# Optimization experiments

Hardware: AMD Instinct MI355X
Metric: run time of the kernel (lower is better)

The kernel has to match this reference:

```python
import jax, jax.numpy as jnp
import numpy as np

RANK = 32
N_ITER = 10
H, W_DIM, C_DIM = 14, 14, 512  # input_shape = (h, w, c)


def _khatri_rao(X, Y):
    # X: [m, r], Y: [n, r] -> [m*n, r], row index = i*n + j (C-order)
    return (X[:, None, :] * Y[None, :, :]).reshape(X.shape[0] * Y.shape[0], X.shape[1])


def _parafac_als(T, key):
    """Rank-RANK CP/ALS decomposition of a single 3-way tensor T [c, h, w].

    Mirrors tensorly.parafac(..., n_iter_max=10, init='random') math:
    per-mode least-squares update factor_n = unfold_n(T) @ KR(others) @ pinv(gram hadamard).
    Returns factors (A [c,r], B [h,r], C [w,r]).
    """
    c, h, w = T.shape
    kA, kB, kC = jax.random.split(key, 3)
    A = jax.random.normal(kA, (c, RANK), dtype=T.dtype)
    B = jax.random.normal(kB, (h, RANK), dtype=T.dtype)
    C = jax.random.normal(kC, (w, RANK), dtype=T.dtype)

    T0 = T.reshape(c, h * w)                      # mode-0 unfolding
    T1 = jnp.transpose(T, (1, 0, 2)).reshape(h, c * w)  # mode-1 unfolding
    T2 = jnp.transpose(T, (2, 0, 1)).reshape(w, c * h)  # mode-2 unfolding

    for _ in range(N_ITER):
        A = T0 @ _khatri_rao(B, C) @ jnp.linalg.pinv((B.T @ B) * (C.T @ C))
        B = T1 @ _khatri_rao(A, C) @ jnp.linalg.pinv((A.T @ A) * (C.T @ C))
        C = T2 @ _khatri_rao(A, B) @ jnp.linalg.pinv((A.T @ A) * (B.T @ B))
    return A, B, C


def setup_inputs() -> dict:
    key = jax.random.key(0)
    k = jax.random.split(key, 5)
    batch = 64
    factor_len = RANK * (H + W_DIM + C_DIM)  # 17280
    hidden = factor_len // 2                 # 8640
    hash_len = 128
    x = jax.random.normal(k[0], (batch, C_DIM, H, W_DIM), dtype=jnp.float32)
    W1 = jax.random.normal(k[1], (hidden, factor_len), dtype=jnp.float32) * (1.0 / np.sqrt(factor_len))
    b1 = jnp.zeros((hidden,), dtype=jnp.float32)
    W2 = jax.random.normal(k[2], (hash_len, hidden), dtype=jnp.float32) * (1.0 / np.sqrt(hidden))
    b2 = jnp.zeros((hash_len,), dtype=jnp.float32)
    return {"x": x, "W1": W1, "b1": b1, "W2": W2, "b2": b2}


def reference(x, W1, b1, W2, b2):
    batch = x.shape[0]
    keys = jax.random.split(jax.random.key(42), batch)
    # batched per-sample CP/ALS (this replaces the Python loop over the batch)
    A, B, C = jax.vmap(_parafac_als)(x, keys)  # [B,c,r], [B,h,r], [B,w,r]
    factor_batch = jnp.concatenate(
        [A.reshape(batch, -1), B.reshape(batch, -1), C.reshape(batch, -1)], axis=1
    )  # [B, rank*(c+h+w)]
    h1 = jax.nn.relu(factor_batch @ W1.T + b1)
    continuous_hash = h1 @ W2.T + b2
    binary_hash = jnp.sign(continuous_hash)  # training STE collapses to sign in fwd
    return binary_hash, continuous_hash
```

## Files before the change

kernel.cpp:

```cpp
#include <hip/hip_runtime.h>
#include <stdint.h>
#include <math.h>

#define RANK 32
#define CDIM 512
#define HD   14
#define WD   14
#define HW   196
#define NITER 10
#define BATCH 64
#define FLEN 17280
#define HID  8640
#define HASH 128
#define NSWEEP 5
#define JSTR 34
#define NPOW_H 5
#define NPOW_I 6
#define KH   3
#define KSEG 5760
#define KT   90

#define A_OFF    0u
#define A_BYTES  8388608u
#define FB_OFF   8388608u
#define FB_BYTES 4423680u
#define BF_OFF   12812288u
#define CF_OFF   13041664u
#define GA_OFF   13271040u
#define P_OFF    13795328u
#define TA_OFF   14319616u
#define RES_OFF  15925248u
#define SENT_OFF 15926784u
#define NFB_OFF  15927040u
#define WS_NEED  15927044u
#define PART_OFF 0u
#define H1_OFF   GA_OFF

#define MAGIC_OK     0x5AFEC0DEu
#define MAGIC_RESBAD 0x0BAD0BADu

#define WSYNC() do { asm volatile("s_waitcnt lgkmcnt(0)" ::: "memory"); \
                     __builtin_amdgcn_wave_barrier(); } while (0)

__device__ __forceinline__ uint32_t rotl32(uint32_t x, int n) {
  return (x << n) | (x >> (32 - n));
}

__device__ __forceinline__ void tf2x32(uint32_t k0, uint32_t k1,
                                       uint32_t x0, uint32_t x1,
                                       uint32_t& y0, uint32_t& y1) {
  uint32_t ks2 = k0 ^ k1 ^ 0x1BD11BDAu;
  x0 += k0; x1 += k1;
#define TFRND(r) { x0 += x1; x1 = rotl32(x1, r); x1 ^= x0; }
  TFRND(13) TFRND(15) TFRND(26) TFRND(6)
  x0 += k1;  x1 += ks2 + 1u;
  TFRND(17) TFRND(29) TFRND(16) TFRND(24)
  x0 += ks2; x1 += k0 + 2u;
  TFRND(13) TFRND(15) TFRND(26) TFRND(6)
  x0 += k0;  x1 += k1 + 3u;
  TFRND(17) TFRND(29) TFRND(16) TFRND(24)
  x0 += k1;  x1 += ks2 + 4u;
  TFRND(13) TFRND(15) TFRND(26) TFRND(6)
  x0 += ks2; x1 += k0 + 5u;
#undef TFRND
  y0 = x0; y1 = x1;
}

__device__ __forceinline__ uint32_t pt_bits(uint32_t k0, uint32_t k1, uint32_t m) {
  uint32_t y0, y1;
  tf2x32(k0, k1, 0u, m, y0, y1);
  return y0 ^ y1;
}
__device__ __forceinline__ void pt_child(uint32_t k0, uint32_t k1, uint32_t i,
                                         uint32_t& c0, uint32_t& c1) {
  tf2x32(k0, k1, 0u, i, c0, c1);
}

__device__ __forceinline__ float erfinv_f32(float x) {
#pragma clang fp contract(off)
  float w = -log1pf(-x * x);
  float p;
  if (w < 5.0f) {
    w = w - 2.5f;
    p = 2.81022636e-08f;
    p = 3.43273939e-07f  + p * w;
    p = -3.5233877e-06f  + p * w;
    p = -4.39150654e-06f + p * w;
    p = 0.00021858087f   + p * w;
    p = -0.00125372503f  + p * w;
    p = -0.00417768164f  + p * w;
    p = 0.246640727f     + p * w;
    p = 1.50140941f      + p * w;
  } else {
    w = sqrtf(w) - 3.0f;
    p = -0.000200214257f;
    p = 0.000100950558f  + p * w;
    p = 0.00134934322f   + p * w;
    p = -0.00367342844f  + p * w;
    p = 0.00573950773f   + p * w;
    p = -0.0076224613f   + p * w;
    p = 0.00943887047f   + p * w;
    p = 1.00167406f      + p * w;
    p = 2.83297682f      + p * w;
  }
  return p * x;
}

__device__ __forceinline__ float nrm_val(uint32_t bits) {
#pragma clang fp contract(off)
  const float lo = -0.99999994f;
  float f = __uint_as_float((bits >> 9) | 0x3f800000u) - 1.0f;
  float u = fmaxf(lo, f * 2.0f + lo);
  return 1.41421356f * erfinv_f32(u);
}

__device__ __forceinline__ void derive_keys(int b,
    uint32_t& a0, uint32_t& a1, uint32_t& b0, uint32_t& b1, uint32_t& c0, uint32_t& c1) {
  uint32_t kb0, kb1;
  pt_child(0u, 42u, (uint32_t)b, kb0, kb1);
  pt_child(kb0, kb1, 0u, a0, a1);
  pt_child(kb0, kb1, 1u, b0, b1);
  pt_child(kb0, kb1, 2u, c0, c1);
}

__global__ __launch_bounds__(512) void init_kernel(double* __restrict__ A,
                                                   double* __restrict__ Bfac,
                                                   double* __restrict__ Cfac) {
  const int b = blockIdx.x, tid = threadIdx.x;
  uint32_t ka0, ka1, kb0, kb1, kc0, kc1;
  derive_keys(b, ka0, ka1, kb0, kb1, kc0, kc1);
  double* Ab = A + (size_t)b * CDIM * RANK;
  for (int m = tid; m < CDIM * RANK; m += 512)
    Ab[m] = (double)nrm_val(pt_bits(ka0, ka1, (uint32_t)m));
  for (int m = tid; m < HD * RANK; m += 512)
    Bfac[b * 448 + m] = (double)nrm_val(pt_bits(kb0, kb1, (uint32_t)m));
  for (int m = tid; m < WD * RANK; m += 512)
    Cfac[b * 448 + m] = (double)nrm_val(pt_bits(kc0, kc1, (uint32_t)m));
}

__device__ double powmax(const double* Hm, double* eigd, int lane, int n) {
  if (lane < 32) eigd[lane] = 1.0 + 0.001 * (double)lane;
  WSYNC();
  double mm = 0.0;
  for (int itp = 0; itp < n; ++itp) {
    double hv = 0.0;
    if (lane < 32) {
      const double* row = &Hm[lane * JSTR];
#pragma unroll 8
      for (int t = 0; t < 32; ++t) hv += row[t] * eigd[t];
    }
    mm = fabs(hv);
#pragma unroll
    for (int off = 1; off < 32; off <<= 1) mm = fmax(mm, __shfl_xor(mm, off));
    WSYNC();
    if (lane < 32) eigd[lane] = hv / mm;
    WSYNC();
  }
  return mm;
}

__device__ __forceinline__ void pq_of(int g, int rr, int& p, int& q) {
  if (g == 0) { p = 31; q = rr; }
  else { p = (rr + g) % 31; q = (rr - g + 31) % 31; }
}

__device__ void jacobi_wave(double* __restrict__ Hm, double* __restrict__ VT,
                            double* __restrict__ eigd, double* __restrict__ rc,
                            double* __restrict__ rs, int lane) {
  for (int e = lane; e < 32 * JSTR; e += 64) VT[e] = 0.0;
  WSYNC();
  if (lane < 32) VT[lane * JSTR + lane] = 1.0;
  WSYNC();
  const int g4   = lane >> 2;
  const int sub  = lane & 3;
  const int jr   = lane & 15;
  const int rowb = (lane >> 4) * 8;
  for (int sw = 0; sw < NSWEEP; ++sw) {
    for (int rr = 0; rr < 31; ++rr) {
      if (lane < 16) {
        int p, q; pq_of(lane, rr, p, q);
        double app = Hm[p * JSTR + p], aqq = Hm[q * JSTR + q], apq = Hm[p * JSTR + q];
        double c = 1.0, s = 0.0;
        if (fabs(apq) > 1e-300) {
          double tau = (aqq - app) / (2.0 * apq);
          double t = ((tau >= 0.0) ? 1.0 : -1.0) / (fabs(tau) + sqrt(1.0 + tau * tau));
          c = 1.0 / sqrt(1.0 + t * t);
          s = t * c;
        }
        rc[lane] = c; rs[lane] = s;
      }
      WSYNC();
      {
        int p, q; pq_of(g4, rr, p, q);
        const double c = rc[g4], s = rs[g4];
        double2* hp = (double2*)&Hm[p * JSTR + sub * 8];
        double2* hq = (double2*)&Hm[q * JSTR + sub * 8];
        double2* vp = (double2*)&VT[p * JSTR + sub * 8];
        double2* vq = (double2*)&VT[q * JSTR + sub * 8];
#pragma unroll
        for (int u = 0; u < 4; ++u) {
          double2 a = hp[u], bb = hq[u];
          hp[u] = make_double2(c * a.x - s * bb.x, c * a.y - s * bb.y);
          hq[u] = make_double2(s * a.x + c * bb.x, s * a.y + c * bb.y);
          double2 va = vp[u], vb = vq[u];
          vp[u] = make_double2(c * va.x - s * vb.x, c * va.y - s * vb.y);
          vq[u] = make_double2(s * va.x + c * vb.x, s * va.y + c * vb.y);
        }
      }
      WSYNC();
      {
        int p, q; pq_of(jr, rr, p, q);
        const double c = rc[jr], s = rs[jr];
#pragma unroll
        for (int u = 0; u < 8; ++u) {
          const int ro = (rowb + u) * JSTR;
          double a = Hm[ro + p], bb = Hm[ro + q];
          Hm[ro + p] = c * a - s * bb;
          Hm[ro + q] = s * a + c * bb;
        }
      }
      WSYNC();
    }
  }
  if (lane == 0) {
    double smax = 0.0;
    for (int i = 0; i < 32; ++i) smax = fmax(smax, fabs(Hm[i * JSTR + i]));
    const double cutoff = 3.814697265625e-05 * smax;
    for (int i = 0; i < 32; ++i) {
      double lam = Hm[i * JSTR + i];
      eigd[i] = (fabs(lam) > cutoff) ? 1.0 / lam : 0.0;
    }
  }
  WSYNC();
}

__device__ void build_H(int which, const double* Bs, const double* Cs,
                        const double* Gab, double* Hm, int lane) {
  for (int t = 0; t < 16; ++t) {
    int e = lane * 16 + t;
    int r1 = e >> 5, r2 = e & 31;
    double h;
    if (which == 0) {
      double sb = 0.0, sc = 0.0;
      for (int i = 0; i < HD; ++i) sb += Bs[i * RANK + r1] * Bs[i * RANK + r2];
      for (int j = 0; j < WD; ++j) sc += Cs[j * RANK + r1] * Cs[j * RANK + r2];
      h = sb * sc;
    } else if (which == 1) {
      double sc = 0.0;
      for (int j = 0; j < WD; ++j) sc += Cs[j * RANK + r1] * Cs[j * RANK + r2];
      h = Gab[e] * sc;
    } else {
      double sb = 0.0;
      for (int i = 0; i < HD; ++i) sb += Bs[i * RANK + r1] * Bs[i * RANK + r2];
      h = Gab[e] * sb;
    }
    Hm[r1 * JSTR + r2] = h;
  }
}

__device__ void pinv_wave_compute(int which, const double* Bs, const double* Cs,
                                  const double* Gab, double* Hm, double* VT,
                                  double* eigd, double* rcs, double* rss,
                                  int lane, unsigned int* nfb) {
  build_H(which, Bs, Cs, Gab, Hm, lane);
  WSYNC();
  double lamH = powmax(Hm, eigd, lane, NPOW_H);
  int bad = 0;
  const int col = lane & 31;
  const int r0  = (lane >> 5) * 16;
  for (int k = 0; k < 32; ++k) {
    double akk = Hm[k * JSTR + k];
    if (!(akk > 0.0)) bad = 1;
    double rk = 1.0 / akk;
    if (lane < 32) {
      double v = Hm[k * JSTR + lane];
      Hm[k * JSTR + lane] = (lane == k) ? rk : v * rk;
    }
    WSYNC();
    double pc = Hm[k * JSTR + col];
    for (int ii = 0; ii < 16; ++ii) {
      int i = r0 + ii;
      if (i == k) continue;
      double f  = Hm[i * JSTR + k];
      double ov = Hm[i * JSTR + col];
      Hm[i * JSTR + col] = (col == k) ? (-f * rk) : (ov - f * pc);
    }
    WSYNC();
  }
  double lamI = powmax(Hm, eigd, lane, NPOW_I);
  int ok = 0;
  if (lane == 0)
    ok = (!bad && (4.0 * 3.814697265625e-05 * lamH * lamI < 1.0)) ? 1 : 0;
  ok = __shfl(ok, 0);
  if (!ok) {
    build_H(which, Bs, Cs, Gab, Hm, lane);
    WSYNC();
    jacobi_wave(Hm, VT, eigd, rcs, rss, lane);
    for (int t = 0; t < 16; ++t) {
      int e = lane * 16 + t;
      int i = e >> 5, j = e & 31;
      double sacc = 0.0;
      for (int kk = 0; kk < 32; ++kk)
        sacc += eigd[kk] * VT[kk * JSTR + i] * VT[kk * JSTR + j];
      Hm[i * JSTR + j] = sacc;
    }
    WSYNC();
    if (lane == 0) atomicAdd(nfb, 1u);
  }
}

__global__ __launch_bounds__(512) void res_pinv_kernel(const float* __restrict__ x,
                                                       const double* __restrict__ A,
                                                       const double* __restrict__ Bfac,
                                                       const double* __restrict__ Cfac,
                                                       double* __restrict__ resbuf,
                                                       double* __restrict__ P,
                                                       unsigned int* __restrict__ nfb) {
  __shared__ float KR[HW * RANK];
  __shared__ double red[512];
  __shared__ double Hm[RANK * JSTR];
  __shared__ double VT[RANK * JSTR];
  __shared__ double Bs[HD * RANK];
  __shared__ double Cs[WD * RANK];
  __shared__ double eigd[RANK];
  __shared__ double rcs[16], rss[16];
  const int tid = threadIdx.x;

  if (blockIdx.x < BATCH) {
    const int b = blockIdx.x;
    const double* Bf = Bfac + b * 448;
    const double* Cf = Cfac + b * 448;
    const double* Ab = A + (size_t)b * CDIM * RANK;
    const float* T0 = x + (size_t)b * CDIM * HW;
    for (int e = tid; e < HW * RANK; e += 512) {
      int ij = e >> 5, r = e & 31;
      KR[e] = (float)(Bf[(ij / WD) * RANK + r] * Cf[(ij % WD) * RANK + r]);
    }
    __syncthreads();
    double areg[32];
    {
      const double2* ar2 = (const double2*)(Ab + (size_t)tid * RANK);
#pragma unroll
      for (int r2 = 0; r2 < 16; ++r2) {
        double2 v = ar2[r2];
        areg[r2 * 2] = v.x;
        areg[r2 * 2 + 1] = v.y;
      }
    }
    double rs = 0.0, nt = 0.0;
    const float4* Trow = (const float4*)(T0 + (size_t)tid * HW);
    for (int q4 = 0; q4 < HW / 4; ++q4) {
      float4 tv = Trow[q4];
#pragma unroll
      for (int u = 0; u < 4; ++u) {
        const int ij = q4 * 4 + u;
        const float4* kr4 = (const float4*)&KR[ij * RANK];
        double f = 0.0;
#pragma unroll
        for (int r4 = 0; r4 < 8; ++r4) {
          float4 kv = kr4[r4];
          f += areg[r4 * 4 + 0] * (double)kv.x;
          f += areg[r4 * 4 + 1] * (double)kv.y;
          f += areg[r4 * 4 + 2] * (double)kv.z;
          f += areg[r4 * 4 + 3] * (double)kv.w;
        }
        double tvd = (double)((const float*)&tv)[u];
        double d = tvd - f;
        rs += d * d; nt += tvd * tvd;
      }
    }
    red[tid] = rs;
    __syncthreads();
    for (int s = 256; s > 0; s >>= 1) {
      if (tid < s) red[tid] += red[tid + s];
      __syncthreads();
    }
    double rsum = red[0];
    __syncthreads();
    red[tid] = nt;
    __syncthreads();
    for (int s = 256; s > 0; s >>= 1) {
      if (tid < s) red[tid] += red[tid + s];
      __syncthreads();
    }
    if (tid == 0) { resbuf[b * 3] = rsum; resbuf[b * 3 + 1] = red[0]; }
  } else {
    const int b = blockIdx.x - BATCH;
    if (tid < 64) {
      const int lane = tid;
      for (int m = lane; m < HD * RANK; m += 64) Bs[m] = Bfac[b * 448 + m];
      for (int m = lane; m < WD * RANK; m += 64) Cs[m] = Cfac[b * 448 + m];
      WSYNC();
      pinv_wave_compute(0, Bs, Cs, nullptr, Hm, VT, eigd, rcs, rss, lane, nfb);
      for (int t = 0; t < 16; ++t) {
        int e = lane * 16 + t;
        P[b * 1024 + e] = Hm[(e >> 5) * JSTR + (e & 31)];
      }
    }
  }
}

__global__ __launch_bounds__(128) void updA_kernel(const float* __restrict__ x,
                                                   const double* __restrict__ Bfac,
                                                   const double* __restrict__ Cfac,
                                                   const double* __restrict__ P,
                                                   double* __restrict__ A) {
  __shared__ float KR[HW * RANK];
  __shared__ double Ps[1024];
  const int b = blockIdx.x >> 2, rb = blockIdx.x & 3;
  const int tid = threadIdx.x;
  const double* Bf = Bfac + b * 448;
  const double* Cf = Cfac + b * 448;
  for (int e = tid; e < HW * RANK; e += 128) {
    int ij = e >> 5, r = e & 31;
    KR[e] = (float)(Bf[(ij / WD) * RANK + r] * Cf[(ij % WD) * RANK + r]);
  }
  for (int e = tid; e < 1024; e += 128) Ps[e] = P[b * 1024 + e];
  __syncthreads();

  const int a = rb * 128 + tid;
  double acc[32];
#pragma unroll
  for (int r = 0; r < 32; ++r) acc[r] = 0.0;
  const float4* Trow = (const float4*)(x + (size_t)b * CDIM * HW + (size_t)a * HW);
  for (int q4 = 0; q4 < HW / 4; ++q4) {
    float4 tv = Trow[q4];
#pragma unroll
    for (int u = 0; u < 4; ++u) {
      double tvd = (double)((const float*)&tv)[u];
      const float4* kr4 = (const float4*)&KR[(q4 * 4 + u) * RANK];
#pragma unroll
      for (int r4 = 0; r4 < 8; ++r4) {
        float4 kv = kr4[r4];
        acc[r4 * 4 + 0] += tvd * (double)kv.x;
        acc[r4 * 4 + 1] += tvd * (double)kv.y;
        acc[r4 * 4 + 2] += tvd * (double)kv.z;
        acc[r4 * 4 + 3] += tvd * (double)kv.w;
      }
    }
  }
  double* Ab = A + (size_t)b * CDIM * RANK + (size_t)a * RANK;
  for (int r = 0; r < 32; ++r) {
    const double2* jrow = (const double2*)&Ps[r * 32];
    double s = 0.0;
#pragma unroll
    for (int k2 = 0; k2 < 16; ++k2) {
      double2 jv = jrow[k2];
      s += jv.x * acc[k2 * 2] + jv.y * acc[k2 * 2 + 1];
    }
    Ab[r] = s;
  }
}

__global__ __launch_bounds__(512) void ga_ta_kernel(const double* __restrict__ A,
                                                    const double* __restrict__ Cfac,
                                                    double* __restrict__ Ga,
                                                    double* __restrict__ P,
                                                    unsigned int* __restrict__ nfb,
                                                    const float* __restrict__ x,
                                                    float* __restrict__ TA) {
  __shared__ double Ach[64 * RANK];
  __shared__ double Gas[1024];
  __shared__ double Cs[WD * RANK];
  __shared__ double Hm[RANK * JSTR];
  __shared__ double VT[RANK * JSTR];
  __shared__ double eigd[RANK];
  __shared__ double rcs[16], rss[16];
  const int tid = threadIdx.x;

  if (blockIdx.x < BATCH) {
    const int b = blockIdx.x;
    const double* Ab = A + (size_t)b * CDIM * RANK;
    for (int m = tid; m < WD * RANK; m += 512) Cs[m] = Cfac[b * 448 + m];
    double g0 = 0.0, g1 = 0.0;
    const int r10 = tid >> 5, r20 = tid & 31;
    const int e1 = tid + 512;
    const int r11 = e1 >> 5, r21 = e1 & 31;
    for (int ch = 0; ch < CDIM / 64; ++ch) {
      for (int e = tid; e < 64 * RANK; e += 512) Ach[e] = Ab[ch * 64 * RANK + e];
      __syncthreads();
      for (int aa = 0; aa < 64; ++aa) {
        const double* ar = &Ach[aa * RANK];
        g0 += ar[r10] * ar[r20];
        g1 += ar[r11] * ar[r21];
      }
      __syncthreads();
    }
    Ga[b * 1024 + tid] = g0;  Gas[tid] = g0;
    Ga[b * 1024 + e1]  = g1;  Gas[e1]  = g1;
    __syncthreads();
    if (tid < 64) {
      pinv_wave_compute(1, nullptr, Cs, Gas, Hm, VT, eigd, rcs, rss, tid, nfb);
      for (int t = 0; t < 16; ++t) {
        int e = tid * 16 + t;
        P[b * 1024 + e] = Hm[(e >> 5) * JSTR + (e & 31)];
      }
    }
  } else {
    const int bb = blockIdx.x - BATCH;
    const int b = bb >> 2, r8 = bb & 3;
    const int ij = tid;
    if (ij >= HW) return;
    const float* T0 = x + (size_t)b * CDIM * HW;
    const double* Ab = A + (size_t)b * CDIM * RANK + r8 * 8;
    double ta[8];
#pragma unroll
    for (int r = 0; r < 8; ++r) ta[r] = 0.0;
    for (int a = 0; a < CDIM; ++a) {
      double tvd = (double)T0[(size_t)a * HW + ij];
      const double2* ap2 = (const double2*)(Ab + (size_t)a * RANK);
#pragma unroll
      for (int r2 = 0; r2 < 4; ++r2) {
        double2 av = ap2[r2];
        ta[r2 * 2]     += tvd * av.x;
        ta[r2 * 2 + 1] += tvd * av.y;
      }
    }
#pragma unroll
    for (int r = 0; r < 8; ++r)
      TA[b * 6272 + ij * RANK + r8 * 8 + r] = (float)ta[r];
  }
}

__global__ __launch_bounds__(512) void updB_pinv2_kernel(const float* __restrict__ TA,
                                                         const double* __restrict__ Cfac,
                                                         const double* __restrict__ Ga,
                                                         double* __restrict__ P,
                                                         double* __restrict__ Bfac,
                                                         unsigned int* __restrict__ nfb) {
  __shared__ double Mt[HD * RANK];
  __shared__ double Cs[WD * RANK];
  __shared__ double Bs[HD * RANK];
  __shared__ double Gas[1024];
  __shared__ double Hm[RANK * JSTR];
  __shared__ double VT[RANK * JSTR];
  __shared__ double eigd[RANK];
  __shared__ double rcs[16], rss[16];
  const int b = blockIdx.x, tid = threadIdx.x;
  const float* TAb = TA + b * 6272;
  for (int m = tid; m < WD * RANK; m += 512) Cs[m] = Cfac[b * 448 + m];
  for (int m = tid; m < 1024; m += 512) Gas[m] = Ga[b * 1024 + m];
  __syncthreads();
  if (tid < HD * RANK) {
    int i = tid >> 5, r = tid & 31;
    double s = 0.0;
    for (int j = 0; j < WD; ++j)
      s += (double)TAb[(i * WD + j) * RANK + r] * Cs[j * RANK + r];
    Mt[tid] = s;
  }
  __syncthreads();
  if (tid < HD) {
    const int i = tid;
    const double* Pb = P + b * 1024;
    for (int r = 0; r < 32; ++r) {
      const double2* jrow = (const double2*)&Pb[r * 32];
      const double2* mrow = (const double2*)&Mt[i * RANK];
      double s = 0.0;
#pragma unroll
      for (int k2 = 0; k2 < 16; ++k2) {
        double2 jv = jrow[k2]; double2 mv = mrow[k2];
        s += jv.x * mv.x + jv.y * mv.y;
      }
      Bs[i * RANK + r] = s;
      Bfac[b * 448 + i * RANK + r] = s;
    }
  }
  __syncthreads();
  if (tid < 64) {
    pinv_wave_compute(2, Bs, nullptr, Gas, Hm, VT, eigd, rcs, rss, tid, nfb);
    for (int t = 0; t < 16; ++t) {
      int e = tid * 16 + t;
      P[b * 1024 + e] = Hm[(e >> 5) * JSTR + (e & 31)];
    }
  }
}

__global__ __launch_bounds__(512) void updC_pinv0_kernel(const float* __restrict__ TA,
                                                         const double* __restrict__ Bfac,
                                                         double* __restrict__ P,
                                                         double* __restrict__ Cfac,
                                                         unsigned int* __restrict__ nfb,
                                                         int do_pinv) {
  __shared__ double Mt[WD * RANK];
  __shared__ double Bs[HD * RANK];
  __shared__ double Cs[WD * RANK];
  __shared__ double Hm[RANK * JSTR];
  __shared__ double VT[RANK * JSTR];
  __shared__ double eigd[RANK];
  __shared__ double rcs[16], rss[16];
  const int b = blockIdx.x, tid = threadIdx.x;
  const float* TAb = TA + b * 6272;
  for (int m = tid; m < HD * RANK; m += 512) Bs[m] = Bfac[b * 448 + m];
  __syncthreads();
  if (tid < WD * RANK) {
    int j = tid >> 5, r = tid & 31;
    double s = 0.0;
    for (int i = 0; i < HD; ++i)
      s += (double)TAb[(i * WD + j) * RANK + r] * Bs[i * RANK + r];
    Mt[tid] = s;
  }
  __syncthreads();
  if (tid < WD) {
    const int j = tid;
    const double* Pb = P + b * 1024;
    for (int r = 0; r < 32; ++r) {
      const double2* jrow = (const double2*)&Pb[r * 32];
      const double2* mrow = (const double2*)&Mt[j * RANK];
      double s = 0.0;
#pragma unroll
      for (int k2 = 0; k2 < 16; ++k2) {
        double2 jv = jrow[k2]; double2 mv = mrow[k2];
        s += jv.x * mv.x + jv.y * mv.y;
      }
      Cs[j * RANK + r] = s;
      Cfac[b * 448 + j * RANK + r] = s;
    }
  }
  __syncthreads();
  if (do_pinv && tid < 64) {
    pinv_wave_compute(0, Bs, Cs, nullptr, Hm, VT, eigd, rcs, rss, tid, nfb);
    for (int t = 0; t < 16; ++t) {
      int e = tid * 16 + t;
      P[b * 1024 + e] = Hm[(e >> 5) * JSTR + (e & 31)];
    }
  }
}

__global__ __launch_bounds__(512) void res_kernel(const float* __restrict__ x,
                                                  const double* __restrict__ A,
                                                  const double* __restrict__ Bfac,
                                                  const double* __restrict__ Cfac,
                                                  double* __restrict__ resbuf,
                                                  uint32_t* __restrict__ sent,
                                                  float* __restrict__ fb) {
  __shared__ float KR[HW * RANK];
  __shared__ double red[512];
  const int b = blockIdx.x, tid = threadIdx.x;
  const double* Bf = Bfac + b * 448;
  const double* Cf = Cfac + b * 448;
  const double* Ab = A + (size_t)b * CDIM * RANK;
  const float* T0 = x + (size_t)b * CDIM * HW;
  for (int e = tid; e < HW * RANK; e += 512) {
    int ij = e >> 5, r = e & 31;
    KR[e] = (float)(Bf[(ij / WD) * RANK + r] * Cf[(ij % WD) * RANK + r]);
  }
  __syncthreads();
  double areg[32];
  {
    const double2* ar2 = (const double2*)(Ab + (size_t)tid * RANK);
#pragma unroll
    for (int r2 = 0; r2 < 16; ++r2) {
      double2 v = ar2[r2];
      areg[r2 * 2] = v.x;
      areg[r2 * 2 + 1] = v.y;
    }
  }
  double rs = 0.0, nt = 0.0;
  const float4* Trow = (const float4*)(T0 + (size_t)tid * HW);
  for (int q4 = 0; q4 < HW / 4; ++q4) {
    float4 tv = Trow[q4];
#pragma unroll
    for (int u = 0; u < 4; ++u) {
      const int ij = q4 * 4 + u;
      const float4* kr4 = (const float4*)&KR[ij * RANK];
      double f = 0.0;
#pragma unroll
      for (int r4 = 0; r4 < 8; ++r4) {
        float4 kv = kr4[r4];
        f += areg[r4 * 4 + 0] * (double)kv.x;
        f += areg[r4 * 4 + 1] * (double)kv.y;
        f += areg[r4 * 4 + 2] * (double)kv.z;
        f += areg[r4 * 4 + 3] * (double)kv.w;
      }
      double tvd = (double)((const float*)&tv)[u];
      double d = tvd - f;
      rs += d * d; nt += tvd * tvd;
    }
  }
  red[tid] = rs;
  __syncthreads();
  for (int s = 256; s > 0; s >>= 1) {
    if (tid < s) red[tid] += red[tid + s];
    __syncthreads();
  }
  double rsum = red[0];
  __syncthreads();
  red[tid] = nt;
  __syncthreads();
  for (int s = 256; s > 0; s >>= 1) {
    if (tid < s) red[tid] += red[tid + s];
    __syncthreads();
  }
  double ntsum = red[0];
  (void)ntsum;

  if (tid == 0)
    sent[b] = (rsum < resbuf[b * 3] && rsum < resbuf[b * 3 + 1]) ? MAGIC_OK : MAGIC_RESBAD;
  float* fbb = fb + (size_t)b * FLEN;
  for (int m = tid; m < CDIM * RANK; m += 512) fbb[m] = (float)Ab[m];
  for (int m = tid; m < HD * RANK; m += 512)
    fbb[CDIM * RANK + m] = (float)Bf[m];
  for (int m = tid; m < WD * RANK; m += 512)
    fbb[CDIM * RANK + HD * RANK + m] = (float)Cf[m];
}

__global__ __launch_bounds__(256) void gemm1_kernel(const float* __restrict__ fb,
                                                    const float* __restrict__ W1,
                                                    float* __restrict__ part) {
  __shared__ __align__(16) float FBs[2][64][72];
  const int cb = blockIdx.x % 135;
  const int kh = blockIdx.x / 135;
  const int t  = threadIdx.x;
  const int cs = t >> 3;
  const int rg = t & 7;
  const int ca = cb * 64 + cs * 2;
  const int cb2 = ca + 1;
  const int srow = t >> 2;
  const int skk  = (t & 3) * 16;
  const int kh0 = kh * KSEG;
  float acc0[8], acc1[8];
#pragma unroll
  for (int r = 0; r < 8; ++r) { acc0[r] = 0.0f; acc1[r] = 0.0f; }

  const float4* src = (const float4*)(fb + (size_t)srow * FLEN + kh0 + skk);
  float4 s0 = src[0], s1 = src[1], s2 = src[2], s3 = src[3];
  int cur = 0;

  for (int kt = 0; kt < KT; ++kt) {
    float (*B)[72] = FBs[cur];
    B[skk + 0][srow]  = s0.x; B[skk + 1][srow]  = s0.y;
    B[skk + 2][srow]  = s0.z; B[skk + 3][srow]  = s0.w;
    B[skk + 4][srow]  = s1.x; B[skk + 5][srow]  = s1.y;
    B[skk + 6][srow]  = s1.z; B[skk + 7][srow]  = s1.w;
    B[skk + 8][srow]  = s2.x; B[skk + 9][srow]  = s2.y;
    B[skk + 10][srow] = s2.z; B[skk + 11][srow] = s2.w;
    B[skk + 12][srow] = s3.x; B[skk + 13][srow] = s3.y;
    B[skk + 14][srow] = s3.z; B[skk + 15][srow] = s3.w;
    __syncthreads();
    if (kt + 1 < KT) {
      src = (const float4*)(fb + (size_t)srow * FLEN + kh0 + (kt + 1) * 64 + skk);
      s0 = src[0]; s1 = src[1]; s2 = src[2]; s3 = src[3];
    }
    const int kbase = kh0 + kt * 64;
    const float4* wa = (const float4*)(W1 + (size_t)ca  * FLEN + kbase);
    const float4* wb = (const float4*)(W1 + (size_t)cb2 * FLEN + kbase);
    for (int k4 = 0; k4 < 16; ++k4) {
      float4 va = wa[k4], vb = wb[k4];
#pragma unroll
      for (int u = 0; u < 4; ++u) {
        const int k = k4 * 4 + u;
        const float fa = ((const float*)&va)[u];
        const float fbv = ((const float*)&vb)[u];
        const float4 f0 = *(const float4*)&B[k][rg * 8];
        const float4 f1 = *(const float4*)&B[k][rg * 8 + 4];
        const float fv[8] = { f0.x, f0.y, f0.z, f0.w, f1.x, f1.y, f1.z, f1.w };
#pragma unroll
        for (int r = 0; r < 8; ++r) {
          acc0[r] += fv[r] * fa;
          acc1[r] += fv[r] * fbv;
        }
      }
    }
    cur ^= 1;
  }
#pragma unroll
  for (int r = 0; r < 8; ++r) {
    const int row = rg * 8 + r;
    part[((size_t)kh * 64 + row) * HID + ca]  = acc0[r];
    part[((size_t)kh * 64 + row) * HID + cb2] = acc1[r];
  }
}

__global__ __launch_bounds__(256) void reduce_relu_kernel(const float* __restrict__ part,
                                                          const float* __restrict__ b1,
                                                          float* __restrict__ h1) {
  const int idx = blockIdx.x * 256 + threadIdx.x;
  if (idx < BATCH * HID) {
    const int col = idx % HID;
    const float v = part[idx] + part[BATCH * HID + idx] + part[2 * BATCH * HID + idx]
                  + b1[col];
    h1[idx] = fmaxf(v, 0.0f);
  }
}

__global__ __launch_bounds__(256) void gemm2_kernel(const float* __restrict__ h1,
                                                    const float* __restrict__ W2,
                                                    const float* __restrict__ b2,
                                                    const unsigned int* __restrict__ nfb,
                                                    float* __restrict__ out) {
  const int gid = blockIdx.x * 256 + threadIdx.x;
  const int bb = gid >> 7, o = gid & 127;
  const float4* hp = (const float4*)(h1 + (size_t)bb * HID);
  const float4* wp = (const float4*)(W2 + (size_t)o * HID);
  double acc = 0.0;
  for (int k4 = 0; k4 < HID / 4; ++k4) {
    float4 hv = hp[k4], wv = wp[k4];
    acc += (double)hv.x * (double)wv.x;
    acc += (double)hv.y * (double)wv.y;
    acc += (double)hv.z * (double)wv.z;
    acc += (double)hv.w * (double)wv.w;
  }
  const double cont = acc + (double)b2[o];
  const float cf = (float)cont;
  unsigned int nt = *nfb;
  const float jit = 2e-3f * (float)(nt < 8u ? nt : 8u);
  const float sg = (cf > 0.0f) ? 1.0f : ((cf < 0.0f) ? -1.0f : 0.0f);
  out[bb * HASH + o] = sg + jit;
  out[BATCH * HASH + bb * HASH + o] = cf;
}

__global__ __launch_bounds__(256) void diag_kernel(const uint32_t* __restrict__ sent,
                                                   float* __restrict__ out) {
  __shared__ int nmiss, nres, Vs;
  const int t = threadIdx.x;
  if (t == 0) { nmiss = 0; nres = 0; }
  __syncthreads();
  if (t < BATCH) {
    uint32_t s = sent[t];
    if (s == MAGIC_RESBAD) atomicAdd(&nres, 1);
    else if (s != MAGIC_OK) atomicAdd(&nmiss, 1);
  }
  __syncthreads();
  if (t == 0) {
    uint32_t y0, y1; int mask = 0;
    tf2x32(0u, 0u, 0u, 0u, y0, y1);
    if (y0 == 0x6b200159u && y1 == 0x99ba4efeu) mask |= 1;
    tf2x32(0xffffffffu, 0xffffffffu, 0xffffffffu, 0xffffffffu, y0, y1);
    if (y0 == 0x1cb996fcu && y1 == 0xbb002be7u) mask |= 2;
    tf2x32(0x13198a2eu, 0x03707344u, 0x243f6a88u, 0x85a308d3u, y0, y1);
    if (y0 == 0xc4923a9cu && y1 == 0x483df7a0u) mask |= 4;
    int V = 0;
    if (nmiss > 0) V = 30;
    else if (nres > 0) V = 40;
    else if (mask != 7) V = 10 + mask;
    Vs = V;
  }
  __syncthreads();
  const int V = Vs;
  if (V > 0) {
    for (int i = t; i < BATCH * HASH; i += 256) out[i] = (float)V;
  }
}

__global__ __launch_bounds__(256) void zero_out_kernel(float* __restrict__ out, int n) {
  const int idx = blockIdx.x * 256 + threadIdx.x;
  if (idx < n) out[idx] = 0.0f;
}

__global__ void init_ctr_kernel(unsigned int* __restrict__ ctr) {
  if (threadIdx.x == 0) *ctr = 0u;
}

extern "C" void kernel_launch(void* const* d_in, const int* in_sizes, int n_in,
                              void* d_out, int out_size, void* d_ws, size_t ws_size,
                              hipStream_t stream) {
  (void)in_sizes; (void)n_in;
  const float* x  = (const float*)d_in[0];
  const float* W1 = (const float*)d_in[1];
  const float* b1 = (const float*)d_in[2];
  const float* W2 = (const float*)d_in[3];
  const float* b2 = (const float*)d_in[4];
  float* out = (float*)d_out;

  if (ws_size < (size_t)WS_NEED) {
    hipLaunchKernelGGL(zero_out_kernel, dim3((out_size + 255) / 256), dim3(256), 0, stream,
                       out, out_size);
    return;
  }

  char* ws = (char*)d_ws;
  double*       A    = (double*)(ws + A_OFF);
  float*        fb   = (float*)(ws + FB_OFF);
  double*       Bfac = (double*)(ws + BF_OFF);
  double*       Cfac = (double*)(ws + CF_OFF);
  double*       Ga   = (double*)(ws + GA_OFF);
  double*       P    = (double*)(ws + P_OFF);
  float*        TA   = (float*)(ws + TA_OFF);
  double*       resb = (double*)(ws + RES_OFF);
  uint32_t*     sent = (uint32_t*)(ws + SENT_OFF);
  unsigned int* nfb  = (unsigned int*)(ws + NFB_OFF);
  float*        part = (float*)(ws + PART_OFF);
  float*        h1   = (float*)(ws + H1_OFF);

  hipLaunchKernelGGL(init_ctr_kernel, dim3(1), dim3(64), 0, stream, nfb);
  hipLaunchKernelGGL(init_kernel, dim3(BATCH), dim3(512), 0, stream, A, Bfac, Cfac);
  hipLaunchKernelGGL(res_pinv_kernel, dim3(2 * BATCH), dim3(512), 0, stream,
                     x, A, Bfac, Cfac, resb, P, nfb);
  for (int it = 0; it < NITER; ++it) {
    hipLaunchKernelGGL(updA_kernel, dim3(BATCH * 4), dim3(128), 0, stream,
                       x, Bfac, Cfac, P, A);
    hipLaunchKernelGGL(ga_ta_kernel, dim3(BATCH + BATCH * 4), dim3(512), 0, stream,
                       A, Cfac, Ga, P, nfb, x, TA);
    hipLaunchKernelGGL(updB_pinv2_kernel, dim3(BATCH), dim3(512), 0, stream,
                       TA, Cfac, Ga, P, Bfac, nfb);
    hipLaunchKernelGGL(updC_pinv0_kernel, dim3(BATCH), dim3(512), 0, stream,
                       TA, Bfac, P, Cfac, nfb, (it < NITER - 1) ? 1 : 0);
  }
  hipLaunchKernelGGL(res_kernel, dim3(BATCH), dim3(512), 0, stream,
                     x, A, Bfac, Cfac, resb, sent, fb);
  hipLaunchKernelGGL(gemm1_kernel, dim3(KH * 135), dim3(256), 0, stream, fb, W1, part);
  hipLaunchKernelGGL(reduce_relu_kernel, dim3((BATCH * HID) / 256), dim3(256), 0, stream,
                     part, b1, h1);
  hipLaunchKernelGGL(gemm2_kernel, dim3((BATCH * HASH) / 256), dim3(256), 0, stream,
                     h1, W2, b2, nfb, out);
  hipLaunchKernelGGL(diag_kernel, dim3(1), dim3(256), 0, stream, sent, out);
}
```

Before: 4.320 ms.

## Fuse B and C factor updates into one kernel; halve gemm1 columns per block

Merges the mode-1 (B) and mode-2 (C) ALS update kernels into a single per-sample kernel. The pinv result computed for the B update is kept in shared memory and reused directly for the C update, which removes one launch per iteration and a global round trip of P and B. Separately, gemm1 now computes one output column per thread instead of two, doubling the grid to 810 blocks. That raises parallelism but reloads the shared feature tile twice as often relative to the useful FMAs.

```diff
diff --git a/kernel.cpp b/kernel.cpp
--- a/kernel.cpp
+++ b/kernel.cpp
@@ -19,6 +19,7 @@
 #define KH   3
 #define KSEG 5760
 #define KT   90
+#define NCB  270
 
 #define A_OFF    0u
 #define A_BYTES  8388608u
@@ -522,12 +523,13 @@
   }
 }
 
-__global__ __launch_bounds__(512) void updB_pinv2_kernel(const float* __restrict__ TA,
-                                                         const double* __restrict__ Cfac,
-                                                         const double* __restrict__ Ga,
-                                                         double* __restrict__ P,
-                                                         double* __restrict__ Bfac,
-                                                         unsigned int* __restrict__ nfb) {
+__global__ __launch_bounds__(512) void updBC_kernel(const float* __restrict__ TA,
+                                                    double* __restrict__ Cfac,
+                                                    const double* __restrict__ Ga,
+                                                    double* __restrict__ P,
+                                                    double* __restrict__ Bfac,
+                                                    unsigned int* __restrict__ nfb,
+                                                    int do_pinv) {
   __shared__ double Mt[HD * RANK];
   __shared__ double Cs[WD * RANK];
   __shared__ double Bs[HD * RANK];
@@ -568,29 +570,10 @@
   __syncthreads();
   if (tid < 64) {
     pinv_wave_compute(2, Bs, nullptr, Gas, Hm, VT, eigd, rcs, rss, tid, nfb);
-    for (int t = 0; t < 16; ++t) {
-      int e = tid * 16 + t;
-      P[b * 1024 + e] = Hm[(e >> 5) * JSTR + (e & 31)];
-    }
-  }
-}
-
-__global__ __launch_bounds__(512) void updC_pinv0_kernel(const float* __restrict__ TA,
-                                                         const double* __restrict__ Bfac,
-                                                         double* __restrict__ P,
-                                                         double* __restrict__ Cfac,
-                                                         unsigned int* __restrict__ nfb,
-                                                         int do_pinv) {
-  __shared__ double Mt[WD * RANK];
-  __shared__ double Bs[HD * RANK];
-  __shared__ double Cs[WD * RANK];
-  __shared__ double Hm[RANK * JSTR];
-  __shared__ double VT[RANK * JSTR];
-  __shared__ double eigd[RANK];
-  __shared__ double rcs[16], rss[16];
-  const int b = blockIdx.x, tid = threadIdx.x;
-  const float* TAb = TA + b * 6272;
-  for (int m = tid; m < HD * RANK; m += 512) Bs[m] = Bfac[b * 448 + m];
+  }
+  __syncthreads();
+  for (int e = tid; e < 1024; e += 512)
+    Gas[e] = Hm[(e >> 5) * JSTR + (e & 31)];
   __syncthreads();
   if (tid < WD * RANK) {
     int j = tid >> 5, r = tid & 31;
@@ -602,9 +585,8 @@
   __syncthreads();
   if (tid < WD) {
     const int j = tid;
-    const double* Pb = P + b * 1024;
     for (int r = 0; r < 32; ++r) {
-      const double2* jrow = (const double2*)&Pb[r * 32];
+      const double2* jrow = (const double2*)&Gas[r * 32];
       const double2* mrow = (const double2*)&Mt[j * RANK];
       double s = 0.0;
 #pragma unroll
@@ -708,19 +690,18 @@
                                                     const float* __restrict__ W1,
                                                     float* __restrict__ part) {
   __shared__ __align__(16) float FBs[2][64][72];
-  const int cb = blockIdx.x % 135;
-  const int kh = blockIdx.x / 135;
+  const int cb = blockIdx.x % NCB;
+  const int kh = blockIdx.x / NCB;
   const int t  = threadIdx.x;
   const int cs = t >> 3;
   const int rg = t & 7;
-  const int ca = cb * 64 + cs * 2;
-  const int cb2 = ca + 1;
+  const int ca = cb * 32 + cs;
   const int srow = t >> 2;
   const int skk  = (t & 3) * 16;
   const int kh0 = kh * KSEG;
-  float acc0[8], acc1[8];
-#pragma unroll
-  for (int r = 0; r < 8; ++r) { acc0[r] = 0.0f; acc1[r] = 0.0f; }
+  float acc0[8];
+#pragma unroll
+  for (int r = 0; r < 8; ++r) acc0[r] = 0.0f;
 
   const float4* src = (const float4*)(fb + (size_t)srow * FLEN + kh0 + skk);
   float4 s0 = src[0], s1 = src[1], s2 = src[2], s3 = src[3];
@@ -742,23 +723,18 @@
       s0 = src[0]; s1 = src[1]; s2 = src[2]; s3 = src[3];
     }
     const int kbase = kh0 + kt * 64;
-    const float4* wa = (const float4*)(W1 + (size_t)ca  * FLEN + kbase);
-    const float4* wb = (const float4*)(W1 + (size_t)cb2 * FLEN + kbase);
+    const float4* wa = (const float4*)(W1 + (size_t)ca * FLEN + kbase);
     for (int k4 = 0; k4 < 16; ++k4) {
-      float4 va = wa[k4], vb = wb[k4];
+      float4 va = wa[k4];
 #pragma unroll
       for (int u = 0; u < 4; ++u) {
         const int k = k4 * 4 + u;
         const float fa = ((const float*)&va)[u];
-        const float fbv = ((const float*)&vb)[u];
         const float4 f0 = *(const float4*)&B[k][rg * 8];
         const float4 f1 = *(const float4*)&B[k][rg * 8 + 4];
         const float fv[8] = { f0.x, f0.y, f0.z, f0.w, f1.x, f1.y, f1.z, f1.w };
 #pragma unroll
-        for (int r = 0; r < 8; ++r) {
-          acc0[r] += fv[r] * fa;
-          acc1[r] += fv[r] * fbv;
-        }
+        for (int r = 0; r < 8; ++r) acc0[r] += fv[r] * fa;
       }
     }
     cur ^= 1;
@@ -766,8 +742,7 @@
 #pragma unroll
   for (int r = 0; r < 8; ++r) {
     const int row = rg * 8 + r;
-    part[((size_t)kh * 64 + row) * HID + ca]  = acc0[r];
-    part[((size_t)kh * 64 + row) * HID + cb2] = acc1[r];
+    part[((size_t)kh * 64 + row) * HID + ca] = acc0[r];
   }
 }
 
@@ -891,14 +866,12 @@
                        x, Bfac, Cfac, P, A);
     hipLaunchKernelGGL(ga_ta_kernel, dim3(BATCH + BATCH * 4), dim3(512), 0, stream,
                        A, Cfac, Ga, P, nfb, x, TA);
-    hipLaunchKernelGGL(updB_pinv2_kernel, dim3(BATCH), dim3(512), 0, stream,
-                       TA, Cfac, Ga, P, Bfac, nfb);
-    hipLaunchKernelGGL(updC_pinv0_kernel, dim3(BATCH), dim3(512), 0, stream,
-                       TA, Bfac, P, Cfac, nfb, (it < NITER - 1) ? 1 : 0);
+    hipLaunchKernelGGL(updBC_kernel, dim3(BATCH), dim3(512), 0, stream,
+                       TA, Cfac, Ga, P, Bfac, nfb, (it < NITER - 1) ? 1 : 0);
   }
   hipLaunchKernelGGL(res_kernel, dim3(BATCH), dim3(512), 0, stream,
                      x, A, Bfac, Cfac, resb, sent, fb);
-  hipLaunchKernelGGL(gemm1_kernel, dim3(KH * 135), dim3(256), 0, stream, fb, W1, part);
+  hipLaunchKernelGGL(gemm1_kernel, dim3(KH * NCB), dim3(256), 0, stream, fb, W1, part);
   hipLaunchKernelGGL(reduce_relu_kernel, dim3((BATCH * HID) / 256), dim3(256), 0, stream,
                      part, b1, h1);
   hipLaunchKernelGGL(gemm2_kernel, dim3((BATCH * HASH) / 256), dim3(256), 0, stream,
```

After: 4.247 ms, median of 3. About the same (-1.7%).
